# Kernel optimization log

Hardware: AMD Instinct MI355X
Metric: run time of the kernel (lower is better)

## Reference

```python
import jax, jax.numpy as jnp
import numpy as np


def setup_inputs() -> dict:
    key = jax.random.key(0)
    ks = jax.random.split(key, 9)
    B, Q, K, F, C = 16, 2048, 2048, 128, 2
    q = jax.random.normal(ks[0], (B, Q, F), dtype=jnp.float32)
    k = jax.random.normal(ks[1], (B, K, F), dtype=jnp.float32)
    v = jax.random.normal(ks[2], (B, K, F), dtype=jnp.float32)
    coords_q = jax.random.uniform(ks[3], (B, Q, C), dtype=jnp.float32)
    coords_k = jax.random.uniform(ks[4], (B, K, C), dtype=jnp.float32)
    attn_mask = jax.random.randint(ks[5], (B, Q, K), 0, 2).astype(jnp.bool_)
    alibi_mask = jax.random.randint(ks[6], (B, Q, K), 0, 2).astype(jnp.bool_)
    bias_scale = jax.random.uniform(ks[7], (1,), dtype=jnp.float32)  # nn.Parameter(torch.rand(1))
    running_mean = jnp.ones((1,), dtype=jnp.float32)  # RunningMeanScaler buffer (eval mode)
    return {"q": q, "k": k, "v": v, "coords_q": coords_q, "coords_k": coords_k,
            "attn_mask": attn_mask, "alibi_mask": alibi_mask,
            "bias_scale": bias_scale, "running_mean": running_mean}


def reference(q, k, v, coords_q, coords_k, attn_mask, alibi_mask, bias_scale, running_mean):
    # [b,q,k] attention logits
    scale = jnp.asarray(k.shape[-1], q.dtype) ** -0.5
    weight_logits = jnp.einsum('bqf,bkf->bqk', q, k) * scale
    # pairwise coordinate distances [b,q,k]
    diff = coords_q[:, :, None, :] - coords_k[:, None, :, :]
    distances = jnp.sqrt(jnp.sum(diff * diff, axis=-1))
    scaled_distances = (distances / running_mean) * bias_scale  # broadcast scalars
    masked_distances = jnp.where(alibi_mask, jnp.zeros((), distances.dtype), scaled_distances)
    weights = jax.nn.softmax(weight_logits, axis=-1)
    masked = jnp.where(attn_mask, jnp.zeros((), weights.dtype), weights - masked_distances)
    attention = jnp.einsum('bqk,bkf->bqf', masked, v)
    return attention
```

## Files before the change

kernel.cpp:

```cpp
#include <hip/hip_runtime.h>
#include <stdint.h>

#define B_  16
#define QL  2048
#define KL  2048
#define FD  128
#define BQ  64
#define BK  32
#define NSTEP (KL/BK)
#define PSTR  40
#define WS_HALF (B_*KL*FD)

typedef __attribute__((ext_vector_type(8))) short bf16x8;
typedef __attribute__((ext_vector_type(4))) float f32x4;

__device__ __forceinline__ unsigned short f2b(float f) {
  union { float f; unsigned u; } x; x.f = f;
  return (unsigned short)((x.u + 0x8000u) >> 16);
}

__global__ __launch_bounds__(256) void conv_k(const float* __restrict__ kp,
                                              unsigned short* __restrict__ kb) {
  int idx = (blockIdx.x * 256 + threadIdx.x) * 4;
  float4 u = *(const float4*)(kp + idx);
  ushort4 s4; s4.x = f2b(u.x); s4.y = f2b(u.y); s4.z = f2b(u.z); s4.w = f2b(u.w);
  *(ushort4*)(kb + idx) = s4;
}

__global__ __launch_bounds__(256) void conv_vt(const float* __restrict__ vp,
                                               unsigned short* __restrict__ vt) {
  __shared__ float tl[32 * 132];
  const int t = threadIdx.x, b = blockIdx.x >> 6, kt = blockIdx.x & 63;
  const int r = t >> 3, f0 = (t & 7) * 16;
  const float* src = vp + ((long long)(b * KL + kt * 32 + r)) * FD + f0;
  #pragma unroll
  for (int i = 0; i < 4; ++i)
    *(float4*)&tl[r * 132 + f0 + 4 * i] = *(const float4*)(src + 4 * i);
  __syncthreads();
  const int f = t >> 1, half = t & 1;
  bf16x8 o0, o1;
  #pragma unroll
  for (int j = 0; j < 8; ++j)  o0[j] = (short)f2b(tl[(half * 16 + j) * 132 + f]);
  #pragma unroll
  for (int j = 0; j < 8; ++j)  o1[j] = (short)f2b(tl[(half * 16 + 8 + j) * 132 + f]);
  unsigned short* dst = vt + ((long long)((b * 64 + kt) * FD + f)) * 32 + half * 16;
  *(bf16x8*)dst = o0;
  *(bf16x8*)(dst + 8) = o1;
}

__global__ __launch_bounds__(256, 2) void alibi_attn(
    const unsigned short* __restrict__ kbp,
    const unsigned short* __restrict__ vtp,
    const float* __restrict__ qp,
    const float* __restrict__ cqp,
    const float* __restrict__ ckp,
    const int* __restrict__ amp,
    const int* __restrict__ almp,
    const float* __restrict__ bsp,
    const float* __restrict__ rmp,
    float* __restrict__ outp)
{
  __shared__ unsigned short plds[4][2][16 * PSTR];

  const int t    = threadIdx.x;
  const int w    = t >> 6;
  const int lane = t & 63;
  const int l15  = lane & 15;
  const int q4   = lane >> 4;

  const int bid  = blockIdx.x;
  const int xcd  = bid & 7, slot = bid >> 3;
  const int b    = (xcd << 1) | (slot >> 5);
  const int qbase = (slot & 31) * BQ;

  const float bscale = bsp[0] / rmp[0];
  const float sl2 = 0.08838834764831845f * 1.44269504089f;

  bf16x8 qfrag[4];
  {
    const float* qrow = qp + ((long long)(b * QL + qbase + w * 16 + l15)) * FD;
    #pragma unroll
    for (int fs = 0; fs < 4; ++fs) {
      float4 u0 = *(const float4*)(qrow + fs * 32 + q4 * 8);
      float4 u1 = *(const float4*)(qrow + fs * 32 + q4 * 8 + 4);
      qfrag[fs][0] = (short)f2b(u0.x); qfrag[fs][1] = (short)f2b(u0.y);
      qfrag[fs][2] = (short)f2b(u0.z); qfrag[fs][3] = (short)f2b(u0.w);
      qfrag[fs][4] = (short)f2b(u1.x); qfrag[fs][5] = (short)f2b(u1.y);
      qfrag[fs][6] = (short)f2b(u1.z); qfrag[fs][7] = (short)f2b(u1.w);
    }
  }
  float cqx[4], cqy[4];
  long long mrow_base[4];
  #pragma unroll
  for (int r = 0; r < 4; ++r) {
    const int qg_ = qbase + w * 16 + q4 * 4 + r;
    float2 c2 = *(const float2*)(cqp + ((long long)(b * QL + qg_)) * 2);
    cqx[r] = c2.x; cqy[r] = c2.y;
    mrow_base[r] = ((long long)(b * QL + qg_)) * KL;
  }

  const unsigned short* kgb = kbp + (long long)b * KL * FD;
  const unsigned short* vgb = vtp + (long long)b * KL * FD;

  int   amv[2][8], alv[2][8];
  float ckxv[2][2], ckyv[2][2];
  #pragma unroll
  for (int s = 0; s < 2; ++s) {
    const int kg = s * 16 + l15;
    #pragma unroll
    for (int r = 0; r < 4; ++r) {
      amv[0][s * 4 + r] = __builtin_nontemporal_load(amp + mrow_base[r] + kg);
      alv[0][s * 4 + r] = __builtin_nontemporal_load(almp + mrow_base[r] + kg);
    }
    float2 c2 = *(const float2*)(ckp + ((long long)(b * KL + kg)) * 2);
    ckxv[0][s] = c2.x; ckyv[0][s] = c2.y;
  }

  f32x4 O1[8], O2[8];
  #pragma unroll
  for (int n = 0; n < 8; ++n) {
    O1[n] = (f32x4){0.f, 0.f, 0.f, 0.f};
    O2[n] = (f32x4){0.f, 0.f, 0.f, 0.f};
  }
  float lsum[4] = {0.f, 0.f, 0.f, 0.f};

  #pragma unroll 2
  for (int kt = 0; kt < NSTEP; ++kt) {
    const int cur = kt & 1, nxt = cur ^ 1;
    const int k0  = kt * BK;
    const int ktp = (kt + 1 < NSTEP) ? (kt + 1) : kt;
    const int k0p = ktp * BK;

    #pragma unroll
    for (int s = 0; s < 2; ++s) {
      const int kg = k0p + s * 16 + l15;
      #pragma unroll
      for (int r = 0; r < 4; ++r) {
        amv[nxt][s * 4 + r] = __builtin_nontemporal_load(amp + mrow_base[r] + kg);
        alv[nxt][s * 4 + r] = __builtin_nontemporal_load(almp + mrow_base[r] + kg);
      }
      float2 c2 = *(const float2*)(ckp + ((long long)(b * KL + kg)) * 2);
      ckxv[nxt][s] = c2.x; ckyv[nxt][s] = c2.y;
    }

    const unsigned short* kt_ptr = kgb + (long long)k0 * FD;
    f32x4 S0 = (f32x4){0.f, 0.f, 0.f, 0.f};
    f32x4 S1 = (f32x4){0.f, 0.f, 0.f, 0.f};
    #pragma unroll
    for (int fs = 0; fs < 4; ++fs) {
      bf16x8 kb0 = *(const bf16x8*)(kt_ptr + (l15)      * FD + fs * 32 + q4 * 8);
      bf16x8 kb1 = *(const bf16x8*)(kt_ptr + (16 + l15) * FD + fs * 32 + q4 * 8);
      S0 = __builtin_amdgcn_mfma_f32_16x16x32_bf16(qfrag[fs], kb0, S0, 0, 0, 0);
      S1 = __builtin_amdgcn_mfma_f32_16x16x32_bf16(qfrag[fs], kb1, S1, 0, 0, 0);
    }

    #pragma unroll
    for (int s = 0; s < 2; ++s) {
      const f32x4 Sv = s ? S1 : S0;
      #pragma unroll
      for (int r = 0; r < 4; ++r) {
        int am = amv[cur][s * 4 + r], al = alv[cur][s * 4 + r];
        float e = __builtin_amdgcn_exp2f(Sv[r] * sl2);
        lsum[r] += e;
        float dx = cqx[r] - ckxv[cur][s], dy = cqy[r] - ckyv[cur][s];
        float d  = sqrtf(fmaf(dx, dx, dy * dy)) * bscale;
        float wv = am ? 0.f : e;
        float tv = (am | al) ? 0.f : d;
        const int mm = q4 * 4 + r, c = s * 16 + l15;
        plds[w][0][mm * PSTR + c] = f2b(wv);
        plds[w][1][mm * PSTR + c] = f2b(tv);
      }
    }

    bf16x8 aw = *(const bf16x8*)&plds[w][0][l15 * PSTR + q4 * 8];
    bf16x8 at = *(const bf16x8*)&plds[w][1][l15 * PSTR + q4 * 8];
    const unsigned short* vt_ptr = vgb + (long long)kt * (BK * FD);
    #pragma unroll
    for (int n = 0; n < 8; ++n) {
      bf16x8 vb = *(const bf16x8*)(vt_ptr + (n * 16 + l15) * 32 + q4 * 8);
      O1[n] = __builtin_amdgcn_mfma_f32_16x16x32_bf16(aw, vb, O1[n], 0, 0, 0);
      O2[n] = __builtin_amdgcn_mfma_f32_16x16x32_bf16(at, vb, O2[n], 0, 0, 0);
    }
  }

  #pragma unroll
  for (int off = 1; off < 16; off <<= 1) {
    #pragma unroll
    for (int r = 0; r < 4; ++r) lsum[r] += __shfl_xor(lsum[r], off, 64);
  }
  float linv[4];
  #pragma unroll
  for (int r = 0; r < 4; ++r) linv[r] = 1.0f / lsum[r];

  #pragma unroll
  for (int n = 0; n < 8; ++n) {
    #pragma unroll
    for (int r = 0; r < 4; ++r) {
      const int qg_ = qbase + w * 16 + q4 * 4 + r;
      const int f   = n * 16 + l15;
      float val = O1[n][r] * linv[r] - O2[n][r];
      __builtin_nontemporal_store(val, outp + ((long long)(b * QL + qg_)) * FD + f);
    }
  }
}

extern "C" void kernel_launch(void* const* d_in, const int* in_sizes, int n_in,
                              void* d_out, int out_size, void* d_ws, size_t ws_size,
                              hipStream_t stream) {
  const float* q   = (const float*)d_in[0];
  const float* k   = (const float*)d_in[1];
  const float* v   = (const float*)d_in[2];
  const float* cq  = (const float*)d_in[3];
  const float* ck  = (const float*)d_in[4];
  const int*   am  = (const int*)d_in[5];
  const int*   alm = (const int*)d_in[6];
  const float* bs  = (const float*)d_in[7];
  const float* rm  = (const float*)d_in[8];
  float*       out = (float*)d_out;

  unsigned short* kb = (unsigned short*)d_ws;
  unsigned short* vt = kb + WS_HALF;

  hipLaunchKernelGGL(conv_k,  dim3(WS_HALF / 1024), dim3(256), 0, stream, k, kb);
  hipLaunchKernelGGL(conv_vt, dim3(B_ * 64),        dim3(256), 0, stream, v, vt);

  dim3 grid(B_ * (QL / BQ));
  dim3 block(256);
  hipLaunchKernelGGL(alibi_attn, grid, block, 0, stream,
                     kb, vt, q, cq, ck, am, alm, bs, rm, out);
}
```

Measured before the change: 800.4 us.

## Stage K and V tiles through double-buffered LDS shared across waves

Before, each of the four waves loaded its own K and V^T fragments straight from global memory, so every tile was fetched four times per block. Now the block loads each bf16 K and V^T tile once into padded LDS, using register prefetch two steps ahead and two LDS buffers, with a barrier at the end of every iteration. Q is also staged through LDS for coalesced conversion into fragments. This cuts global and L2 traffic but adds about 35KB of LDS per block, a barrier per step and more registers, which could hurt occupancy at the 2-block launch bound.

```diff
diff --git a/kernel.cpp b/kernel.cpp
--- a/kernel.cpp
+++ b/kernel.cpp
@@ -8,6 +8,11 @@
 #define BQ  64
 #define BK  32
 #define NSTEP (KL/BK)
+
+#define KSTR  136
+#define VTOFF 4352
+#define VTSTR 36
+#define BUFS  8960
 #define PSTR  40
 #define WS_HALF (B_*KL*FD)
 
@@ -60,6 +65,7 @@
     const float* __restrict__ rmp,
     float* __restrict__ outp)
 {
+  __shared__ unsigned short kv[2 * BUFS];
   __shared__ unsigned short plds[4][2][16 * PSTR];
 
   const int t    = threadIdx.x;
@@ -76,18 +82,27 @@
   const float bscale = bsp[0] / rmp[0];
   const float sl2 = 0.08838834764831845f * 1.44269504089f;
 
+  const int kr_st = t >> 3, kc_st = (t & 7) * 16;
+  const int vf_st = t >> 1, vh_st = (t & 1) * 16;
+
+  {
+    const float* qg = qp + ((long long)(b * QL + qbase)) * FD;
+    #pragma unroll
+    for (int i = 0; i < 8; ++i) {
+      int idx = t + 256 * i;
+      float4 u = ((const float4*)qg)[idx];
+      int row = idx >> 5, col = (idx & 31) * 4;
+      ushort4 s4; s4.x = f2b(u.x); s4.y = f2b(u.y); s4.z = f2b(u.z); s4.w = f2b(u.w);
+      *(ushort4*)&kv[row * KSTR + col] = s4;
+    }
+  }
+  __syncthreads();
   bf16x8 qfrag[4];
   {
-    const float* qrow = qp + ((long long)(b * QL + qbase + w * 16 + l15)) * FD;
-    #pragma unroll
-    for (int fs = 0; fs < 4; ++fs) {
-      float4 u0 = *(const float4*)(qrow + fs * 32 + q4 * 8);
-      float4 u1 = *(const float4*)(qrow + fs * 32 + q4 * 8 + 4);
-      qfrag[fs][0] = (short)f2b(u0.x); qfrag[fs][1] = (short)f2b(u0.y);
-      qfrag[fs][2] = (short)f2b(u0.z); qfrag[fs][3] = (short)f2b(u0.w);
-      qfrag[fs][4] = (short)f2b(u1.x); qfrag[fs][5] = (short)f2b(u1.y);
-      qfrag[fs][6] = (short)f2b(u1.z); qfrag[fs][7] = (short)f2b(u1.w);
-    }
+    const int m = w * 16 + l15;
+    #pragma unroll
+    for (int fs = 0; fs < 4; ++fs)
+      qfrag[fs] = *(const bf16x8*)&kv[m * KSTR + fs * 32 + q4 * 8];
   }
   float cqx[4], cqy[4];
   long long mrow_base[4];
@@ -98,12 +113,14 @@
     cqx[r] = c2.x; cqy[r] = c2.y;
     mrow_base[r] = ((long long)(b * QL + qg_)) * KL;
   }
+  __syncthreads();
 
   const unsigned short* kgb = kbp + (long long)b * KL * FD;
   const unsigned short* vgb = vtp + (long long)b * KL * FD;
 
   int   amv[2][8], alv[2][8];
   float ckxv[2][2], ckyv[2][2];
+  bf16x8 kreg[2][2], vreg[2][2];
   #pragma unroll
   for (int s = 0; s < 2; ++s) {
     const int kg = s * 16 + l15;
@@ -115,6 +132,21 @@
     float2 c2 = *(const float2*)(ckp + ((long long)(b * KL + kg)) * 2);
     ckxv[0][s] = c2.x; ckyv[0][s] = c2.y;
   }
+  {
+    bf16x8 k0l = *(const bf16x8*)(kgb + kr_st * FD + kc_st);
+    bf16x8 k1l = *(const bf16x8*)(kgb + kr_st * FD + kc_st + 8);
+    bf16x8 v0l = *(const bf16x8*)(vgb + t * 16);
+    bf16x8 v1l = *(const bf16x8*)(vgb + t * 16 + 8);
+    *(bf16x8*)&kv[kr_st * KSTR + kc_st]     = k0l;
+    *(bf16x8*)&kv[kr_st * KSTR + kc_st + 8] = k1l;
+    *(bf16x8*)&kv[VTOFF + vf_st * VTSTR + vh_st]     = v0l;
+    *(bf16x8*)&kv[VTOFF + vf_st * VTSTR + vh_st + 8] = v1l;
+    kreg[1][0] = *(const bf16x8*)(kgb + (BK + kr_st) * FD + kc_st);
+    kreg[1][1] = *(const bf16x8*)(kgb + (BK + kr_st) * FD + kc_st + 8);
+    vreg[1][0] = *(const bf16x8*)(vgb + BK * FD + t * 16);
+    vreg[1][1] = *(const bf16x8*)(vgb + BK * FD + t * 16 + 8);
+  }
+  __syncthreads();
 
   f32x4 O1[8], O2[8];
   #pragma unroll
@@ -127,13 +159,19 @@
   #pragma unroll 2
   for (int kt = 0; kt < NSTEP; ++kt) {
     const int cur = kt & 1, nxt = cur ^ 1;
-    const int k0  = kt * BK;
-    const int ktp = (kt + 1 < NSTEP) ? (kt + 1) : kt;
-    const int k0p = ktp * BK;
-
+    const unsigned short* kb = kv + cur * BUFS;
+    unsigned short*       nb = kv + nxt * BUFS;
+
+    const int ktf = (kt + 2 < NSTEP) ? (kt + 2) : (NSTEP - 1);
+    kreg[cur][0] = *(const bf16x8*)(kgb + (ktf * BK + kr_st) * FD + kc_st);
+    kreg[cur][1] = *(const bf16x8*)(kgb + (ktf * BK + kr_st) * FD + kc_st + 8);
+    vreg[cur][0] = *(const bf16x8*)(vgb + ktf * (BK * FD) + t * 16);
+    vreg[cur][1] = *(const bf16x8*)(vgb + ktf * (BK * FD) + t * 16 + 8);
+
+    const int ktm = (kt + 1 < NSTEP) ? (kt + 1) : kt;
     #pragma unroll
     for (int s = 0; s < 2; ++s) {
-      const int kg = k0p + s * 16 + l15;
+      const int kg = ktm * BK + s * 16 + l15;
       #pragma unroll
       for (int r = 0; r < 4; ++r) {
         amv[nxt][s * 4 + r] = __builtin_nontemporal_load(amp + mrow_base[r] + kg);
@@ -143,13 +181,12 @@
       ckxv[nxt][s] = c2.x; ckyv[nxt][s] = c2.y;
     }
 
-    const unsigned short* kt_ptr = kgb + (long long)k0 * FD;
     f32x4 S0 = (f32x4){0.f, 0.f, 0.f, 0.f};
     f32x4 S1 = (f32x4){0.f, 0.f, 0.f, 0.f};
     #pragma unroll
     for (int fs = 0; fs < 4; ++fs) {
-      bf16x8 kb0 = *(const bf16x8*)(kt_ptr + (l15)      * FD + fs * 32 + q4 * 8);
-      bf16x8 kb1 = *(const bf16x8*)(kt_ptr + (16 + l15) * FD + fs * 32 + q4 * 8);
+      bf16x8 kb0 = *(const bf16x8*)&kb[(l15)      * KSTR + fs * 32 + q4 * 8];
+      bf16x8 kb1 = *(const bf16x8*)&kb[(16 + l15) * KSTR + fs * 32 + q4 * 8];
       S0 = __builtin_amdgcn_mfma_f32_16x16x32_bf16(qfrag[fs], kb0, S0, 0, 0, 0);
       S1 = __builtin_amdgcn_mfma_f32_16x16x32_bf16(qfrag[fs], kb1, S1, 0, 0, 0);
     }
@@ -174,13 +211,19 @@
 
     bf16x8 aw = *(const bf16x8*)&plds[w][0][l15 * PSTR + q4 * 8];
     bf16x8 at = *(const bf16x8*)&plds[w][1][l15 * PSTR + q4 * 8];
-    const unsigned short* vt_ptr = vgb + (long long)kt * (BK * FD);
     #pragma unroll
     for (int n = 0; n < 8; ++n) {
-      bf16x8 vb = *(const bf16x8*)(vt_ptr + (n * 16 + l15) * 32 + q4 * 8);
+      bf16x8 vb = *(const bf16x8*)&kb[VTOFF + (n * 16 + l15) * VTSTR + q4 * 8];
       O1[n] = __builtin_amdgcn_mfma_f32_16x16x32_bf16(aw, vb, O1[n], 0, 0, 0);
       O2[n] = __builtin_amdgcn_mfma_f32_16x16x32_bf16(at, vb, O2[n], 0, 0, 0);
     }
+
+    *(bf16x8*)&nb[kr_st * KSTR + kc_st]     = kreg[nxt][0];
+    *(bf16x8*)&nb[kr_st * KSTR + kc_st + 8] = kreg[nxt][1];
+    *(bf16x8*)&nb[VTOFF + vf_st * VTSTR + vh_st]     = vreg[nxt][0];
+    *(bf16x8*)&nb[VTOFF + vf_st * VTSTR + vh_st + 8] = vreg[nxt][1];
+
+    asm volatile("s_waitcnt lgkmcnt(0)\n\ts_barrier" ::: "memory");
   }
 
   #pragma unroll
```

Measured after the change: 660.8 us. 1.21x faster.
